# Performance work log

Measured on AMD Instinct MI355X. Metric: run time of the kernel, lower is better.

The kernel has to match this reference:

```python
import jax, jax.numpy as jnp
import numpy as np

IN_FEATURES = 16384
OUT_FEATURES = 16384
NNZ = 1_000_000
BATCH = 256


def setup_inputs() -> dict:
    key = jax.random.key(0)
    k1, k2, k3 = jax.random.split(key, 3)
    x = jax.random.normal(k1, (IN_FEATURES, BATCH), dtype=jnp.float32)
    values = jax.random.normal(k2, (NNZ,), dtype=jnp.float32)
    indices = jax.random.randint(k3, (2, NNZ), 0, OUT_FEATURES, dtype=jnp.int64)
    bias = jnp.zeros((OUT_FEATURES, 1), dtype=jnp.float32)
    return {"x": x, "values": values, "indices": indices, "bias": bias}


def reference(x, values, indices, bias):
    # Sparse (COO) matmul: out[r, :] += values[k] * x[c, :] for each nnz (r, c).
    # Equivalent to torch.sparse.mm(W_coo.coalesce(), x) + bias since
    # coalesce() sums duplicate entries and segment_sum does the same.
    row = indices[0]  # [nnz] in [0, OUT_FEATURES)
    col = indices[1]  # [nnz] in [0, IN_FEATURES)
    gathered = values[:, None] * x[col]  # [nnz, B]
    out = jax.ops.segment_sum(gathered, row, num_segments=OUT_FEATURES)  # [out, B]
    return out + bias
```

## Files before the change

kernel.cpp:

```cpp
#include <hip/hip_runtime.h>

typedef unsigned int u32;
typedef unsigned short u16;

constexpr int OUT_F = 16384;
constexpr int IN_F  = 16384;
constexpr int B_N   = 256;
constexpr int NGRP  = 256;
constexpr int GCAP  = 4608;
constexpr int BINB  = 4096;


__global__ __launch_bounds__(1024) void prep_k(
    const int* __restrict__ rows, const int* __restrict__ cols,
    const float* __restrict__ vals, const float* __restrict__ x,
    u16* __restrict__ xb, int* __restrict__ gcnt,
    uint2* __restrict__ gbuck, int nnz, int nbin, int n4) {
  const int tid = threadIdx.x;

  if ((int)blockIdx.x >= nbin) {
    const int i2 = blockIdx.x - nbin;
    for (int j = 0; j < 4; ++j) {
      int k4 = i2 * 4096 + j * 1024 + tid;
      if (k4 < n4) {
        float4 v = ((const float4*)x)[k4];
        u32 u0 = __float_as_uint(v.x), u1 = __float_as_uint(v.y),
            u2 = __float_as_uint(v.z), u3 = __float_as_uint(v.w);
        ushort4 r;
        r.x = (u16)((u0 + 0x7FFFu + ((u0 >> 16) & 1u)) >> 16);
        r.y = (u16)((u1 + 0x7FFFu + ((u1 >> 16) & 1u)) >> 16);
        r.z = (u16)((u2 + 0x7FFFu + ((u2 >> 16) & 1u)) >> 16);
        r.w = (u16)((u3 + 0x7FFFu + ((u3 >> 16) & 1u)) >> 16);
        ((ushort4*)xb)[k4] = r;
      }
    }
    return;
  }

  __shared__ int   hist[NGRP], lofs[NGRP], cur[NGRP], gbase[NGRP], scanb[NGRP];
  __shared__ uint2 stage[BINB];
  __shared__ int   tgt[BINB];

  const int base = blockIdx.x * BINB;
  const int nval = min(BINB, nnz - base);
  if (tid < NGRP) hist[tid] = 0;
  __syncthreads();

  int r[4]; u32 c[4]; float v[4]; bool ok[4];
#pragma unroll
  for (int i = 0; i < 4; ++i) {
    int k = base + i * 1024 + tid;
    ok[i] = k < nnz;
    if (ok[i]) {
      r[i] = rows[k]; c[i] = (u32)cols[k]; v[i] = vals[k];
      atomicAdd(&hist[r[i] >> 6], 1);
    }
  }
  __syncthreads();

  if (tid < NGRP) scanb[tid] = hist[tid];
  __syncthreads();
  for (int off = 1; off < NGRP; off <<= 1) {
    int t = 0;
    if (tid < NGRP && tid >= off) t = scanb[tid - off];
    __syncthreads();
    if (tid < NGRP) scanb[tid] += t;
    __syncthreads();
  }
  if (tid < NGRP) {
    int lo = scanb[tid] - hist[tid];
    lofs[tid] = lo;
    cur[tid]  = lo;
    gbase[tid] = atomicAdd(&gcnt[tid], hist[tid]);
  }
  __syncthreads();

#pragma unroll
  for (int i = 0; i < 4; ++i) {
    if (ok[i]) {
      int g   = r[i] >> 6;
      int pos = atomicAdd(&cur[g], 1);
      stage[pos].x = (c[i] << 6) | (u32)(r[i] & 63);
      stage[pos].y = __float_as_uint(v[i]);
      int w = gbase[g] + (pos - lofs[g]);
      tgt[pos] = (w < GCAP) ? (g * GCAP + w) : -1;
    }
  }
  __syncthreads();

#pragma unroll
  for (int j = 0; j < 4; ++j) {
    int idx = j * 1024 + tid;
    if (idx < nval) {
      int t = tgt[idx];
      if (t >= 0) gbuck[t] = stage[idx];
    }
  }
}

__global__ __launch_bounds__(1024) void regroup_k(
    int* __restrict__ gcnt, uint2* __restrict__ gbuck,
    int* __restrict__ rowstart, int* __restrict__ rowcnt) {
  __shared__ int hist[4096];
  __shared__ int part[1024];
  const int tid = threadIdx.x;
  const int g   = blockIdx.x;
  int cnt = gcnt[g];
  if (cnt > GCAP) cnt = GCAP;
  uint2* bk  = gbuck + (size_t)g * GCAP;
  u32*  pk32 = (u32*)gbuck + (size_t)g * GCAP;

#pragma unroll
  for (int i = 0; i < 4; ++i) hist[i * 1024 + tid] = 0;
  __syncthreads();

  uint2 e[5]; int bin[5]; bool ok[5];
#pragma unroll
  for (int i = 0; i < 5; ++i) {
    int k = i * 1024 + tid;
    ok[i] = k < cnt;
    if (ok[i]) {
      e[i] = bk[k];
      bin[i] = (int)(((e[i].x & 63u) << 6) | ((e[i].x >> 6) >> 8));
      atomicAdd(&hist[bin[i]], 1);
    }
  }
  __syncthreads();

  int loc[4]; int s = 0;
#pragma unroll
  for (int i = 0; i < 4; ++i) { loc[i] = hist[tid * 4 + i]; s += loc[i]; }
  part[tid] = s;
  __syncthreads();
  for (int off = 1; off < 1024; off <<= 1) {
    int t = (tid >= off) ? part[tid - off] : 0;
    __syncthreads();
    part[tid] += t;
    __syncthreads();
  }
  int run = (tid == 0) ? 0 : part[tid - 1];
  __syncthreads();
#pragma unroll
  for (int i = 0; i < 4; ++i) { hist[tid * 4 + i] = run; run += loc[i]; }
  __syncthreads();

  if (tid < 64) {
    int lo = hist[tid << 6];
    int hi = (tid == 63) ? cnt : hist[(tid + 1) << 6];
    rowstart[g * 64 + tid] = g * GCAP + lo;
    rowcnt[g * 64 + tid]   = hi - lo;
  }
  __syncthreads();

#pragma unroll
  for (int i = 0; i < 5; ++i) {
    if (ok[i]) {
      int pos = atomicAdd(&hist[bin[i]], 1);
      u32 col = e[i].x >> 6;
      pk32[pos] = (col << 18) | (e[i].y >> 14);
    }
  }
}

__global__ __launch_bounds__(256) void spmm_final_k(
    const int* __restrict__ rowstart, const int* __restrict__ rowcnt,
    const u32* __restrict__ gpk, const u16* __restrict__ xb,
    const float* __restrict__ bias, float* __restrict__ out) {
  const int lane = threadIdx.x & 63;
  const int wid  = threadIdx.x >> 6;
  const int r    = blockIdx.x * 4 + wid;
  const int cnt  = rowcnt[r];
  const u32* bk  = gpk + rowstart[r];
  float a0 = 0.f, a1 = 0.f, a2 = 0.f, a3 = 0.f;
  for (int base = 0; base < cnt; base += 64) {
    const int m = min(64, cnt - base);
    u32 pk = 0;
    if (lane < m) pk = bk[base + lane];
    int j = 0;
    for (; j + 8 <= m; j += 8) {
      u32 e0 = (u32)__builtin_amdgcn_readlane((int)pk, j);
      u32 e1 = (u32)__builtin_amdgcn_readlane((int)pk, j + 1);
      u32 e2 = (u32)__builtin_amdgcn_readlane((int)pk, j + 2);
      u32 e3 = (u32)__builtin_amdgcn_readlane((int)pk, j + 3);
      u32 e4 = (u32)__builtin_amdgcn_readlane((int)pk, j + 4);
      u32 e5 = (u32)__builtin_amdgcn_readlane((int)pk, j + 5);
      u32 e6 = (u32)__builtin_amdgcn_readlane((int)pk, j + 6);
      u32 e7 = (u32)__builtin_amdgcn_readlane((int)pk, j + 7);
      uint2 x0 = ((const uint2*)(xb + ((size_t)(e0 >> 18) << 8)))[lane];
      uint2 x1 = ((const uint2*)(xb + ((size_t)(e1 >> 18) << 8)))[lane];
      uint2 x2 = ((const uint2*)(xb + ((size_t)(e2 >> 18) << 8)))[lane];
      uint2 x3 = ((const uint2*)(xb + ((size_t)(e3 >> 18) << 8)))[lane];
      uint2 x4 = ((const uint2*)(xb + ((size_t)(e4 >> 18) << 8)))[lane];
      uint2 x5 = ((const uint2*)(xb + ((size_t)(e5 >> 18) << 8)))[lane];
      uint2 x6 = ((const uint2*)(xb + ((size_t)(e6 >> 18) << 8)))[lane];
      uint2 x7 = ((const uint2*)(xb + ((size_t)(e7 >> 18) << 8)))[lane];
      float v0 = __uint_as_float(e0 << 14), v1 = __uint_as_float(e1 << 14);
      float v2 = __uint_as_float(e2 << 14), v3 = __uint_as_float(e3 << 14);
      float v4 = __uint_as_float(e4 << 14), v5 = __uint_as_float(e5 << 14);
      float v6 = __uint_as_float(e6 << 14), v7 = __uint_as_float(e7 << 14);
      a0 = fmaf(v0, __uint_as_float(x0.x << 16), a0);
      a1 = fmaf(v0, __uint_as_float(x0.x & 0xFFFF0000u), a1);
      a2 = fmaf(v0, __uint_as_float(x0.y << 16), a2);
      a3 = fmaf(v0, __uint_as_float(x0.y & 0xFFFF0000u), a3);
      a0 = fmaf(v1, __uint_as_float(x1.x << 16), a0);
      a1 = fmaf(v1, __uint_as_float(x1.x & 0xFFFF0000u), a1);
      a2 = fmaf(v1, __uint_as_float(x1.y << 16), a2);
      a3 = fmaf(v1, __uint_as_float(x1.y & 0xFFFF0000u), a3);
      a0 = fmaf(v2, __uint_as_float(x2.x << 16), a0);
      a1 = fmaf(v2, __uint_as_float(x2.x & 0xFFFF0000u), a1);
      a2 = fmaf(v2, __uint_as_float(x2.y << 16), a2);
      a3 = fmaf(v2, __uint_as_float(x2.y & 0xFFFF0000u), a3);
      a0 = fmaf(v3, __uint_as_float(x3.x << 16), a0);
      a1 = fmaf(v3, __uint_as_float(x3.x & 0xFFFF0000u), a1);
      a2 = fmaf(v3, __uint_as_float(x3.y << 16), a2);
      a3 = fmaf(v3, __uint_as_float(x3.y & 0xFFFF0000u), a3);
      a0 = fmaf(v4, __uint_as_float(x4.x << 16), a0);
      a1 = fmaf(v4, __uint_as_float(x4.x & 0xFFFF0000u), a1);
      a2 = fmaf(v4, __uint_as_float(x4.y << 16), a2);
      a3 = fmaf(v4, __uint_as_float(x4.y & 0xFFFF0000u), a3);
      a0 = fmaf(v5, __uint_as_float(x5.x << 16), a0);
      a1 = fmaf(v5, __uint_as_float(x5.x & 0xFFFF0000u), a1);
      a2 = fmaf(v5, __uint_as_float(x5.y << 16), a2);
      a3 = fmaf(v5, __uint_as_float(x5.y & 0xFFFF0000u), a3);
      a0 = fmaf(v6, __uint_as_float(x6.x << 16), a0);
      a1 = fmaf(v6, __uint_as_float(x6.x & 0xFFFF0000u), a1);
      a2 = fmaf(v6, __uint_as_float(x6.y << 16), a2);
      a3 = fmaf(v6, __uint_as_float(x6.y & 0xFFFF0000u), a3);
      a0 = fmaf(v7, __uint_as_float(x7.x << 16), a0);
      a1 = fmaf(v7, __uint_as_float(x7.x & 0xFFFF0000u), a1);
      a2 = fmaf(v7, __uint_as_float(x7.y << 16), a2);
      a3 = fmaf(v7, __uint_as_float(x7.y & 0xFFFF0000u), a3);
    }
    for (; j < m; ++j) {
      u32 e = (u32)__builtin_amdgcn_readlane((int)pk, j);
      float v = __uint_as_float(e << 14);
      uint2 xx = ((const uint2*)(xb + ((size_t)(e >> 18) << 8)))[lane];
      a0 = fmaf(v, __uint_as_float(xx.x << 16), a0);
      a1 = fmaf(v, __uint_as_float(xx.x & 0xFFFF0000u), a1);
      a2 = fmaf(v, __uint_as_float(xx.y << 16), a2);
      a3 = fmaf(v, __uint_as_float(xx.y & 0xFFFF0000u), a3);
    }
  }
  const float bv = bias[r];
  float4 o;
  o.x = a0 + bv; o.y = a1 + bv; o.z = a2 + bv; o.w = a3 + bv;
  ((float4*)(out + (size_t)r * B_N))[lane] = o;
}


__global__ __launch_bounds__(256) void hist_k(const int* __restrict__ rows,
                                              int* __restrict__ counts, int nnz) {
  int k = blockIdx.x * 256 + threadIdx.x;
  if (k < nnz) atomicAdd(&counts[rows[k]], 1);
}

__global__ __launch_bounds__(1024) void scan_k(const int* __restrict__ counts,
                                               int* __restrict__ offsets,
                                               int* __restrict__ cursor) {
  __shared__ int part[1024];
  const int tid  = threadIdx.x;
  const int base = tid * 16;
  int loc[16];
  int s = 0;
#pragma unroll
  for (int i = 0; i < 16; ++i) { loc[i] = counts[base + i]; s += loc[i]; }
  part[tid] = s;
  __syncthreads();
  for (int off = 1; off < 1024; off <<= 1) {
    int v = (tid >= off) ? part[tid - off] : 0;
    __syncthreads();
    part[tid] += v;
    __syncthreads();
  }
  int run = (tid == 0) ? 0 : part[tid - 1];
#pragma unroll
  for (int i = 0; i < 16; ++i) {
    offsets[base + i] = run;
    cursor[base + i]  = run;
    run += loc[i];
  }
  if (tid == 1023) offsets[OUT_F] = run;
}

__global__ __launch_bounds__(256) void scatter_k(const int* __restrict__ rows,
                                                 const int* __restrict__ colsIn,
                                                 const float* __restrict__ vals,
                                                 int* __restrict__ cursor,
                                                 int* __restrict__ colsOut,
                                                 float* __restrict__ valsOut,
                                                 int nnz) {
  int k = blockIdx.x * 256 + threadIdx.x;
  if (k < nnz) {
    int r   = rows[k];
    int pos = atomicAdd(&cursor[r], 1);
    colsOut[pos] = colsIn[k];
    valsOut[pos] = vals[k];
  }
}

__global__ __launch_bounds__(256) void spmm_k(const int* __restrict__ offsets,
                                              const int* __restrict__ cols,
                                              const float* __restrict__ vals,
                                              const float* __restrict__ x,
                                              const float* __restrict__ bias,
                                              float* __restrict__ out) {
  __shared__ int   c_lds[256];
  __shared__ float v_lds[256];
  const int r = blockIdx.x;
  const int b = threadIdx.x;
  const int start = offsets[r];
  const int end   = offsets[r + 1];
  float acc = 0.f;
  for (int basei = start; basei < end; basei += 256) {
    const int n = min(256, end - basei);
    if (threadIdx.x < n) {
      c_lds[threadIdx.x] = cols[basei + threadIdx.x];
      v_lds[threadIdx.x] = vals[basei + threadIdx.x];
    }
    __syncthreads();
    for (int j = 0; j < n; ++j) {
      acc = fmaf(v_lds[j], x[(size_t)c_lds[j] * B_N + b], acc);
    }
    __syncthreads();
  }
  out[(size_t)r * B_N + b] = acc + bias[r];
}


__global__ __launch_bounds__(256) void initout_k(const float* __restrict__ bias,
                                                 float* __restrict__ out) {
  int i = blockIdx.x * 256 + threadIdx.x;
  out[i] = bias[i >> 8];
}

__global__ __launch_bounds__(256) void atomic_k(const int* __restrict__ rows,
                                                const int* __restrict__ colsIn,
                                                const float* __restrict__ vals,
                                                const float* __restrict__ x,
                                                float* __restrict__ out, int nnz) {
  int k = blockIdx.x;
  if (k < nnz) {
    int r = rows[k], c = colsIn[k];
    float v = vals[k];
    int b = threadIdx.x;
    atomicAdd(&out[(size_t)r * B_N + b], v * x[(size_t)c * B_N + b]);
  }
}

extern "C" void kernel_launch(void* const* d_in, const int* in_sizes, int n_in,
                              void* d_out, int out_size, void* d_ws, size_t ws_size,
                              hipStream_t stream) {
  const float* x      = (const float*)d_in[0];
  const float* values = (const float*)d_in[1];
  const int*   idx    = (const int*)d_in[2];
  const float* bias   = (const float*)d_in[3];
  float* out = (float*)d_out;

  const int nnz = in_sizes[2] / 2;
  const int* rows   = idx;
  const int* colsIn = idx + nnz;

  char* ws = (char*)d_ws;
  auto align256 = [](size_t v) { return (v + 255) & ~(size_t)255; };

  size_t t1_gcnt  = 0;
  size_t t1_rs    = align256(t1_gcnt + (size_t)NGRP * 4);
  size_t t1_rc    = align256(t1_rs + (size_t)OUT_F * 4);
  size_t t1_gbuck = align256(t1_rc + (size_t)OUT_F * 4);
  size_t t1_xb    = align256(t1_gbuck + (size_t)NGRP * GCAP * 8);
  size_t t1_need  = align256(t1_xb + (size_t)IN_F * B_N * 2);

  size_t t2_counts  = 0;
  size_t t2_offsets = align256(t2_counts + (size_t)OUT_F * 4);
  size_t t2_cursor  = align256(t2_offsets + ((size_t)OUT_F + 1) * 4);
  size_t t2_cols    = align256(t2_cursor + (size_t)OUT_F * 4);
  size_t t2_vals    = align256(t2_cols + (size_t)nnz * 4);
  size_t t2_need    = align256(t2_vals + (size_t)nnz * 4);

  if (ws_size >= t1_need) {
    int*   gcnt     = (int*)(ws + t1_gcnt);
    int*   rowstart = (int*)(ws + t1_rs);
    int*   rowcnt   = (int*)(ws + t1_rc);
    uint2* gbuck    = (uint2*)(ws + t1_gbuck);
    u16*   xb       = (u16*)(ws + t1_xb);

    const int n4   = IN_F * B_N / 4;
    const int nbin = (nnz + BINB - 1) / BINB;
    const int nxc  = (n4 + 4095) / 4096;

    hipMemsetAsync(gcnt, 0, (size_t)NGRP * 4, stream);
    prep_k<<<nbin + nxc, 1024, 0, stream>>>(rows, colsIn, values, x, xb, gcnt,
                                            gbuck, nnz, nbin, n4);
    regroup_k<<<NGRP, 1024, 0, stream>>>(gcnt, gbuck, rowstart, rowcnt);
    spmm_final_k<<<OUT_F / 4, 256, 0, stream>>>(rowstart, rowcnt, (const u32*)gbuck,
                                                xb, bias, out);
  } else if (ws_size >= t2_need) {
    int*   counts  = (int*)(ws + t2_counts);
    int*   offsets = (int*)(ws + t2_offsets);
    int*   cursor  = (int*)(ws + t2_cursor);
    int*   colsB   = (int*)(ws + t2_cols);
    float* valsB   = (float*)(ws + t2_vals);

    const int nblk = (nnz + 255) / 256;
    hipMemsetAsync(counts, 0, (size_t)OUT_F * 4, stream);
    hist_k<<<nblk, 256, 0, stream>>>(rows, counts, nnz);
    scan_k<<<1, 1024, 0, stream>>>(counts, offsets, cursor);
    scatter_k<<<nblk, 256, 0, stream>>>(rows, colsIn, values, cursor, colsB, valsB, nnz);
    spmm_k<<<OUT_F, 256, 0, stream>>>(offsets, colsB, valsB, x, bias, out);
  } else {
    initout_k<<<(out_size + 255) / 256, 256, 0, stream>>>(bias, out);
    atomic_k<<<nnz, 256, 0, stream>>>(rows, colsIn, values, x, out, nnz);
  }
}
```

Baseline: 77.91 us.

## Fuse regroup sort and SpMM into one kernel using LDS-resident packed entries

Merges the per-group counting sort and the row SpMM into a single kernel. Sorted packed entries and row offsets stay in shared memory instead of going through global memory, and each 1024-thread block processes its 64 rows, four per wavefront. This removes one launch and a global write/read of the packed buffer. The cost is far fewer, larger blocks for the gather phase, which reduces parallelism and may hurt load balance and latency hiding.

```diff
diff --git a/kernel.cpp b/kernel.cpp
--- a/kernel.cpp
+++ b/kernel.cpp
@@ -98,17 +98,19 @@
   }
 }
 
-__global__ __launch_bounds__(1024) void regroup_k(
-    int* __restrict__ gcnt, uint2* __restrict__ gbuck,
-    int* __restrict__ rowstart, int* __restrict__ rowcnt) {
+__global__ __launch_bounds__(1024) void sortspmm_k(
+    const int* __restrict__ gcnt, const uint2* __restrict__ gbuck,
+    const u16* __restrict__ xb, const float* __restrict__ bias,
+    float* __restrict__ out) {
   __shared__ int hist[4096];
   __shared__ int part[1024];
+  __shared__ u32 pk_lds[GCAP];
+  __shared__ int rs[64], rc[64];
   const int tid = threadIdx.x;
   const int g   = blockIdx.x;
   int cnt = gcnt[g];
   if (cnt > GCAP) cnt = GCAP;
-  uint2* bk  = gbuck + (size_t)g * GCAP;
-  u32*  pk32 = (u32*)gbuck + (size_t)g * GCAP;
+  const uint2* bk = gbuck + (size_t)g * GCAP;
 
 #pragma unroll
   for (int i = 0; i < 4; ++i) hist[i * 1024 + tid] = 0;
@@ -147,8 +149,8 @@
   if (tid < 64) {
     int lo = hist[tid << 6];
     int hi = (tid == 63) ? cnt : hist[(tid + 1) << 6];
-    rowstart[g * 64 + tid] = g * GCAP + lo;
-    rowcnt[g * 64 + tid]   = hi - lo;
+    rs[tid] = lo;
+    rc[tid] = hi - lo;
   }
   __syncthreads();
 
@@ -157,94 +159,95 @@
     if (ok[i]) {
       int pos = atomicAdd(&hist[bin[i]], 1);
       u32 col = e[i].x >> 6;
-      pk32[pos] = (col << 18) | (e[i].y >> 14);
-    }
-  }
-}
-
-__global__ __launch_bounds__(256) void spmm_final_k(
-    const int* __restrict__ rowstart, const int* __restrict__ rowcnt,
-    const u32* __restrict__ gpk, const u16* __restrict__ xb,
-    const float* __restrict__ bias, float* __restrict__ out) {
-  const int lane = threadIdx.x & 63;
-  const int wid  = threadIdx.x >> 6;
-  const int r    = blockIdx.x * 4 + wid;
-  const int cnt  = rowcnt[r];
-  const u32* bk  = gpk + rowstart[r];
-  float a0 = 0.f, a1 = 0.f, a2 = 0.f, a3 = 0.f;
-  for (int base = 0; base < cnt; base += 64) {
-    const int m = min(64, cnt - base);
-    u32 pk = 0;
-    if (lane < m) pk = bk[base + lane];
-    int j = 0;
-    for (; j + 8 <= m; j += 8) {
-      u32 e0 = (u32)__builtin_amdgcn_readlane((int)pk, j);
-      u32 e1 = (u32)__builtin_amdgcn_readlane((int)pk, j + 1);
-      u32 e2 = (u32)__builtin_amdgcn_readlane((int)pk, j + 2);
-      u32 e3 = (u32)__builtin_amdgcn_readlane((int)pk, j + 3);
-      u32 e4 = (u32)__builtin_amdgcn_readlane((int)pk, j + 4);
-      u32 e5 = (u32)__builtin_amdgcn_readlane((int)pk, j + 5);
-      u32 e6 = (u32)__builtin_amdgcn_readlane((int)pk, j + 6);
-      u32 e7 = (u32)__builtin_amdgcn_readlane((int)pk, j + 7);
-      uint2 x0 = ((const uint2*)(xb + ((size_t)(e0 >> 18) << 8)))[lane];
-      uint2 x1 = ((const uint2*)(xb + ((size_t)(e1 >> 18) << 8)))[lane];
-      uint2 x2 = ((const uint2*)(xb + ((size_t)(e2 >> 18) << 8)))[lane];
-      uint2 x3 = ((const uint2*)(xb + ((size_t)(e3 >> 18) << 8)))[lane];
-      uint2 x4 = ((const uint2*)(xb + ((size_t)(e4 >> 18) << 8)))[lane];
-      uint2 x5 = ((const uint2*)(xb + ((size_t)(e5 >> 18) << 8)))[lane];
-      uint2 x6 = ((const uint2*)(xb + ((size_t)(e6 >> 18) << 8)))[lane];
-      uint2 x7 = ((const uint2*)(xb + ((size_t)(e7 >> 18) << 8)))[lane];
-      float v0 = __uint_as_float(e0 << 14), v1 = __uint_as_float(e1 << 14);
-      float v2 = __uint_as_float(e2 << 14), v3 = __uint_as_float(e3 << 14);
-      float v4 = __uint_as_float(e4 << 14), v5 = __uint_as_float(e5 << 14);
-      float v6 = __uint_as_float(e6 << 14), v7 = __uint_as_float(e7 << 14);
-      a0 = fmaf(v0, __uint_as_float(x0.x << 16), a0);
-      a1 = fmaf(v0, __uint_as_float(x0.x & 0xFFFF0000u), a1);
-      a2 = fmaf(v0, __uint_as_float(x0.y << 16), a2);
-      a3 = fmaf(v0, __uint_as_float(x0.y & 0xFFFF0000u), a3);
-      a0 = fmaf(v1, __uint_as_float(x1.x << 16), a0);
-      a1 = fmaf(v1, __uint_as_float(x1.x & 0xFFFF0000u), a1);
-      a2 = fmaf(v1, __uint_as_float(x1.y << 16), a2);
-      a3 = fmaf(v1, __uint_as_float(x1.y & 0xFFFF0000u), a3);
-      a0 = fmaf(v2, __uint_as_float(x2.x << 16), a0);
-      a1 = fmaf(v2, __uint_as_float(x2.x & 0xFFFF0000u), a1);
-      a2 = fmaf(v2, __uint_as_float(x2.y << 16), a2);
-      a3 = fmaf(v2, __uint_as_float(x2.y & 0xFFFF0000u), a3);
-      a0 = fmaf(v3, __uint_as_float(x3.x << 16), a0);
-      a1 = fmaf(v3, __uint_as_float(x3.x & 0xFFFF0000u), a1);
-      a2 = fmaf(v3, __uint_as_float(x3.y << 16), a2);
-      a3 = fmaf(v3, __uint_as_float(x3.y & 0xFFFF0000u), a3);
-      a0 = fmaf(v4, __uint_as_float(x4.x << 16), a0);
-      a1 = fmaf(v4, __uint_as_float(x4.x & 0xFFFF0000u), a1);
-      a2 = fmaf(v4, __uint_as_float(x4.y << 16), a2);
-      a3 = fmaf(v4, __uint_as_float(x4.y & 0xFFFF0000u), a3);
-      a0 = fmaf(v5, __uint_as_float(x5.x << 16), a0);
-      a1 = fmaf(v5, __uint_as_float(x5.x & 0xFFFF0000u), a1);
-      a2 = fmaf(v5, __uint_as_float(x5.y << 16), a2);
-      a3 = fmaf(v5, __uint_as_float(x5.y & 0xFFFF0000u), a3);
-      a0 = fmaf(v6, __uint_as_float(x6.x << 16), a0);
-      a1 = fmaf(v6, __uint_as_float(x6.x & 0xFFFF0000u), a1);
-      a2 = fmaf(v6, __uint_as_float(x6.y << 16), a2);
-      a3 = fmaf(v6, __uint_as_float(x6.y & 0xFFFF0000u), a3);
-      a0 = fmaf(v7, __uint_as_float(x7.x << 16), a0);
-      a1 = fmaf(v7, __uint_as_float(x7.x & 0xFFFF0000u), a1);
-      a2 = fmaf(v7, __uint_as_float(x7.y << 16), a2);
-      a3 = fmaf(v7, __uint_as_float(x7.y & 0xFFFF0000u), a3);
-    }
-    for (; j < m; ++j) {
-      u32 e = (u32)__builtin_amdgcn_readlane((int)pk, j);
-      float v = __uint_as_float(e << 14);
-      uint2 xx = ((const uint2*)(xb + ((size_t)(e >> 18) << 8)))[lane];
-      a0 = fmaf(v, __uint_as_float(xx.x << 16), a0);
-      a1 = fmaf(v, __uint_as_float(xx.x & 0xFFFF0000u), a1);
-      a2 = fmaf(v, __uint_as_float(xx.y << 16), a2);
-      a3 = fmaf(v, __uint_as_float(xx.y & 0xFFFF0000u), a3);
-    }
-  }
-  const float bv = bias[r];
-  float4 o;
-  o.x = a0 + bv; o.y = a1 + bv; o.z = a2 + bv; o.w = a3 + bv;
-  ((float4*)(out + (size_t)r * B_N))[lane] = o;
+      pk_lds[pos] = (col << 18) | (e[i].y >> 14);
+    }
+  }
+  __syncthreads();
+
+  const int lane = tid & 63;
+  const int wid  = tid >> 6;
+  const int r0g  = g * 64;
+
+  for (int rr = 0; rr < 4; ++rr) {
+    const int fr   = wid * 4 + rr;
+    const int st   = rs[fr];
+    const int cntr = rc[fr];
+    float a0 = 0.f, a1 = 0.f, a2 = 0.f, a3 = 0.f;
+    for (int base = 0; base < cntr; base += 64) {
+      const int m = min(64, cntr - base);
+      u32 pk = 0;
+      if (lane < m) pk = pk_lds[st + base + lane];
+      int j = 0;
+      for (; j + 8 <= m; j += 8) {
+        u32 e0 = (u32)__builtin_amdgcn_readlane((int)pk, j);
+        u32 e1 = (u32)__builtin_amdgcn_readlane((int)pk, j + 1);
+        u32 e2 = (u32)__builtin_amdgcn_readlane((int)pk, j + 2);
+        u32 e3 = (u32)__builtin_amdgcn_readlane((int)pk, j + 3);
+        u32 e4 = (u32)__builtin_amdgcn_readlane((int)pk, j + 4);
+        u32 e5 = (u32)__builtin_amdgcn_readlane((int)pk, j + 5);
+        u32 e6 = (u32)__builtin_amdgcn_readlane((int)pk, j + 6);
+        u32 e7 = (u32)__builtin_amdgcn_readlane((int)pk, j + 7);
+        uint2 x0 = ((const uint2*)(xb + ((size_t)(e0 >> 18) << 8)))[lane];
+        uint2 x1 = ((const uint2*)(xb + ((size_t)(e1 >> 18) << 8)))[lane];
+        uint2 x2 = ((const uint2*)(xb + ((size_t)(e2 >> 18) << 8)))[lane];
+        uint2 x3 = ((const uint2*)(xb + ((size_t)(e3 >> 18) << 8)))[lane];
+        uint2 x4 = ((const uint2*)(xb + ((size_t)(e4 >> 18) << 8)))[lane];
+        uint2 x5 = ((const uint2*)(xb + ((size_t)(e5 >> 18) << 8)))[lane];
+        uint2 x6 = ((const uint2*)(xb + ((size_t)(e6 >> 18) << 8)))[lane];
+        uint2 x7 = ((const uint2*)(xb + ((size_t)(e7 >> 18) << 8)))[lane];
+        float v0 = __uint_as_float(e0 << 14), v1 = __uint_as_float(e1 << 14);
+        float v2 = __uint_as_float(e2 << 14), v3 = __uint_as_float(e3 << 14);
+        float v4 = __uint_as_float(e4 << 14), v5 = __uint_as_float(e5 << 14);
+        float v6 = __uint_as_float(e6 << 14), v7 = __uint_as_float(e7 << 14);
+        a0 = fmaf(v0, __uint_as_float(x0.x << 16), a0);
+        a1 = fmaf(v0, __uint_as_float(x0.x & 0xFFFF0000u), a1);
+        a2 = fmaf(v0, __uint_as_float(x0.y << 16), a2);
+        a3 = fmaf(v0, __uint_as_float(x0.y & 0xFFFF0000u), a3);
+        a0 = fmaf(v1, __uint_as_float(x1.x << 16), a0);
+        a1 = fmaf(v1, __uint_as_float(x1.x & 0xFFFF0000u), a1);
+        a2 = fmaf(v1, __uint_as_float(x1.y << 16), a2);
+        a3 = fmaf(v1, __uint_as_float(x1.y & 0xFFFF0000u), a3);
+        a0 = fmaf(v2, __uint_as_float(x2.x << 16), a0);
+        a1 = fmaf(v2, __uint_as_float(x2.x & 0xFFFF0000u), a1);
+        a2 = fmaf(v2, __uint_as_float(x2.y << 16), a2);
+        a3 = fmaf(v2, __uint_as_float(x2.y & 0xFFFF0000u), a3);
+        a0 = fmaf(v3, __uint_as_float(x3.x << 16), a0);
+        a1 = fmaf(v3, __uint_as_float(x3.x & 0xFFFF0000u), a1);
+        a2 = fmaf(v3, __uint_as_float(x3.y << 16), a2);
+        a3 = fmaf(v3, __uint_as_float(x3.y & 0xFFFF0000u), a3);
+        a0 = fmaf(v4, __uint_as_float(x4.x << 16), a0);
+        a1 = fmaf(v4, __uint_as_float(x4.x & 0xFFFF0000u), a1);
+        a2 = fmaf(v4, __uint_as_float(x4.y << 16), a2);
+        a3 = fmaf(v4, __uint_as_float(x4.y & 0xFFFF0000u), a3);
+        a0 = fmaf(v5, __uint_as_float(x5.x << 16), a0);
+        a1 = fmaf(v5, __uint_as_float(x5.x & 0xFFFF0000u), a1);
+        a2 = fmaf(v5, __uint_as_float(x5.y << 16), a2);
+        a3 = fmaf(v5, __uint_as_float(x5.y & 0xFFFF0000u), a3);
+        a0 = fmaf(v6, __uint_as_float(x6.x << 16), a0);
+        a1 = fmaf(v6, __uint_as_float(x6.x & 0xFFFF0000u), a1);
+        a2 = fmaf(v6, __uint_as_float(x6.y << 16), a2);
+        a3 = fmaf(v6, __uint_as_float(x6.y & 0xFFFF0000u), a3);
+        a0 = fmaf(v7, __uint_as_float(x7.x << 16), a0);
+        a1 = fmaf(v7, __uint_as_float(x7.x & 0xFFFF0000u), a1);
+        a2 = fmaf(v7, __uint_as_float(x7.y << 16), a2);
+        a3 = fmaf(v7, __uint_as_float(x7.y & 0xFFFF0000u), a3);
+      }
+      for (; j < m; ++j) {
+        u32 ee = (u32)__builtin_amdgcn_readlane((int)pk, j);
+        float v = __uint_as_float(ee << 14);
+        uint2 xx = ((const uint2*)(xb + ((size_t)(ee >> 18) << 8)))[lane];
+        a0 = fmaf(v, __uint_as_float(xx.x << 16), a0);
+        a1 = fmaf(v, __uint_as_float(xx.x & 0xFFFF0000u), a1);
+        a2 = fmaf(v, __uint_as_float(xx.y << 16), a2);
+        a3 = fmaf(v, __uint_as_float(xx.y & 0xFFFF0000u), a3);
+      }
+    }
+    const int rout = r0g + fr;
+    const float bv = bias[rout];
+    float4 o;
+    o.x = a0 + bv; o.y = a1 + bv; o.z = a2 + bv; o.w = a3 + bv;
+    ((float4*)(out + (size_t)rout * B_N))[lane] = o;
+  }
 }
 
 
@@ -364,9 +367,7 @@
   auto align256 = [](size_t v) { return (v + 255) & ~(size_t)255; };
 
   size_t t1_gcnt  = 0;
-  size_t t1_rs    = align256(t1_gcnt + (size_t)NGRP * 4);
-  size_t t1_rc    = align256(t1_rs + (size_t)OUT_F * 4);
-  size_t t1_gbuck = align256(t1_rc + (size_t)OUT_F * 4);
+  size_t t1_gbuck = align256(t1_gcnt + (size_t)NGRP * 4);
   size_t t1_xb    = align256(t1_gbuck + (size_t)NGRP * GCAP * 8);
   size_t t1_need  = align256(t1_xb + (size_t)IN_F * B_N * 2);
 
@@ -378,11 +379,9 @@
   size_t t2_need    = align256(t2_vals + (size_t)nnz * 4);
 
   if (ws_size >= t1_need) {
-    int*   gcnt     = (int*)(ws + t1_gcnt);
-    int*   rowstart = (int*)(ws + t1_rs);
-    int*   rowcnt   = (int*)(ws + t1_rc);
-    uint2* gbuck    = (uint2*)(ws + t1_gbuck);
-    u16*   xb       = (u16*)(ws + t1_xb);
+    int*   gcnt  = (int*)(ws + t1_gcnt);
+    uint2* gbuck = (uint2*)(ws + t1_gbuck);
+    u16*   xb    = (u16*)(ws + t1_xb);
 
     const int n4   = IN_F * B_N / 4;
     const int nbin = (nnz + BINB - 1) / BINB;
@@ -391,9 +390,7 @@
     hipMemsetAsync(gcnt, 0, (size_t)NGRP * 4, stream);
     prep_k<<<nbin + nxc, 1024, 0, stream>>>(rows, colsIn, values, x, xb, gcnt,
                                             gbuck, nnz, nbin, n4);
-    regroup_k<<<NGRP, 1024, 0, stream>>>(gcnt, gbuck, rowstart, rowcnt);
-    spmm_final_k<<<OUT_F / 4, 256, 0, stream>>>(rowstart, rowcnt, (const u32*)gbuck,
-                                                xb, bias, out);
+    sortspmm_k<<<NGRP, 1024, 0, stream>>>(gcnt, gbuck, xb, bias, out);
   } else if (ws_size >= t2_need) {
     int*   counts  = (int*)(ws + t2_counts);
     int*   offsets = (int*)(ws + t2_offsets);
```

After: 71.99 us. -7.6%, faster.
